# Kernel tuning notes

Hardware: AMD Instinct MI355X
Metric: run time of the kernel (lower is better)

## Reference

```python
import jax, jax.numpy as jnp
import numpy as np

EMBED_DIM = 1024
HEADS = 16
HD = EMBED_DIM // HEADS

def setup_inputs() -> dict:
    key = jax.random.key(0)
    ks = jax.random.split(key, 6)
    s = 1.0 / np.sqrt(EMBED_DIM)
    x = jax.random.normal(ks[0], (4, 2048, EMBED_DIM), dtype=jnp.float32)
    Wq = jax.random.uniform(ks[1], (EMBED_DIM, EMBED_DIM), jnp.float32, -s, s)
    Wk = jax.random.uniform(ks[2], (EMBED_DIM, EMBED_DIM), jnp.float32, -s, s)
    Wv = jax.random.uniform(ks[3], (EMBED_DIM, EMBED_DIM), jnp.float32, -s, s)
    Wo = jax.random.uniform(ks[4], (EMBED_DIM, EMBED_DIM), jnp.float32, -s, s)
    bo = jax.random.uniform(ks[5], (EMBED_DIM,), jnp.float32, -s, s)
    return {"x": x, "Wq": Wq, "Wk": Wk, "Wv": Wv, "Wo": Wo, "bo": bo}

def reference(x, Wq, Wk, Wv, Wo, bo):
    B, S, E = x.shape
    # projections (torch Linear: y = x @ W.T), split into heads -> [B,H,S,hd]
    def proj(W):
        return (x @ W.T).reshape(B, S, HEADS, HD).transpose(0, 2, 1, 3)
    q, k, v = proj(Wq), proj(Wk), proj(Wv)
    energy = jnp.einsum('bhid,bhjd->bhij', q, k) / np.sqrt(HD).astype(np.float32)
    causal = jnp.tril(jnp.ones((S, S), dtype=bool))
    energy = jnp.where(causal, energy, -jnp.inf)
    attn = jax.nn.softmax(energy, axis=-1)  # dropout omitted (eval mode)
    out = jnp.einsum('bhij,bhjd->bhid', attn, v)
    out = out.transpose(0, 2, 1, 3).reshape(B, S, E)
    return out @ Wo.T + bo
```

## Files before the change

kernel.cpp:

```cpp
#include <hip/hip_runtime.h>
#include <math.h>

#define EMB   1024
#define HEADS 16
#define HD    64
#define SEQ   2048
#define BATCH 4
#define MTOT  (BATCH * SEQ)
#define XSZ   ((size_t)MTOT * EMB)
#define WSZ   ((size_t)EMB * EMB)

typedef __attribute__((ext_vector_type(8))) short s16x8;
typedef __attribute__((ext_vector_type(4))) short s16x4;
typedef __attribute__((ext_vector_type(4))) float f32x4;

__device__ __forceinline__ short f2bf(float f) {
    unsigned u = __builtin_bit_cast(unsigned, f);
    u += 0x7fffu + ((u >> 16) & 1u);
    return (short)(u >> 16);
}

__device__ __forceinline__ unsigned pk_bf16(float a, float b) {
#if __has_builtin(__builtin_amdgcn_cvt_pk_bf16_f32)
    typedef __attribute__((ext_vector_type(2))) __bf16 bf16x2;
    return __builtin_bit_cast(unsigned, __builtin_amdgcn_cvt_pk_bf16_f32(a, b));
#else
    return (unsigned)(unsigned short)f2bf(a) |
           ((unsigned)(unsigned short)f2bf(b) << 16);
#endif
}

__device__ __forceinline__ float fexp2(float x) {
#if __has_builtin(__builtin_amdgcn_exp2f)
    return __builtin_amdgcn_exp2f(x);
#else
    return exp2f(x);
#endif
}

__device__ __forceinline__ void async16(const void* g, void* l) {
    __builtin_amdgcn_global_load_lds(
        (const __attribute__((address_space(1))) unsigned*)g,
        (__attribute__((address_space(3))) unsigned*)l, 16, 0, 0);
}

__global__ __launch_bounds__(256)
void cvt_inputs(const float* __restrict__ x,  const float* __restrict__ wq,
                const float* __restrict__ wk, const float* __restrict__ wv,
                const float* __restrict__ wo, short* __restrict__ xb,
                short* __restrict__ wcat)
{
    const size_t e = ((size_t)blockIdx.x * 256 + threadIdx.x) * 8;
    const float* src;
    short* dst;
    float scale = 1.0f;
    if (e < XSZ) {
        src = x + e;
        dst = xb + e;
    } else {
        const size_t r = e - XSZ;
        const int w = (int)(r >> 20);
        const size_t off = r & (WSZ - 1);
        src = (w == 0 ? wq : w == 1 ? wk : w == 2 ? wv : wo) + off;
        dst = wcat + r;
        if (w == 0) scale = 0.125f * 1.44269504f;
    }
    const float4 a = ((const float4*)src)[0];
    const float4 b = ((const float4*)src)[1];
    s16x8 v;
    v[0] = f2bf(a.x * scale); v[1] = f2bf(a.y * scale);
    v[2] = f2bf(a.z * scale); v[3] = f2bf(a.w * scale);
    v[4] = f2bf(b.x * scale); v[5] = f2bf(b.y * scale);
    v[6] = f2bf(b.z * scale); v[7] = f2bf(b.w * scale);
    *(s16x8*)dst = v;
}

#define BAR() __builtin_amdgcn_s_barrier()
#define WAIT_LGKM() do { asm volatile("s_waitcnt lgkmcnt(0)" ::: "memory"); \
                         __builtin_amdgcn_sched_barrier(0); } while (0)
#define WAIT_VM(n) asm volatile("s_waitcnt vmcnt(" #n ")" ::: "memory")

#define RD_A4(bA) \
    _Pragma("unroll") for (int mi = 0; mi < 4; ++mi) \
    _Pragma("unroll") for (int kk = 0; kk < 2; ++kk) \
        a[mi][kk] = *(const s16x8*)((bA) + (wm4 + mi) * 2048 + kk * 1024 + abase);

#define RD_B2(bB, hf, breg) \
    _Pragma("unroll") for (int ni = 0; ni < 2; ++ni) \
    _Pragma("unroll") for (int kk = 0; kk < 2; ++kk) \
        breg[ni][kk] = *(const s16x8*)((bB) + (wn4 + (hf) * 2 + ni) * 2048 + kk * 1024 + abase);

#define MFMA16(hf, breg) \
    __builtin_amdgcn_s_setprio(1); \
    _Pragma("unroll") for (int mi = 0; mi < 4; ++mi) \
    _Pragma("unroll") for (int ni = 0; ni < 2; ++ni) \
    _Pragma("unroll") for (int kk = 0; kk < 2; ++kk) \
        acc[mi][(hf) * 2 + ni] = __builtin_amdgcn_mfma_f32_16x16x32_bf16( \
            a[mi][kk], breg[ni][kk], acc[mi][(hf) * 2 + ni], 0, 0, 0); \
    __builtin_amdgcn_s_setprio(0);

#define STA(pM, ldsM, h, k0) do { \
    async16((pM) + (size_t)((h) * 128) * K + (k0),      (ldsM) + (h) * 16384 + wv1024); \
    async16((pM) + (size_t)((h) * 128 + 64) * K + (k0), (ldsM) + (h) * 16384 + 8192 + wv1024); \
} while (0)

#define STB(pM, ldsM, k0) do { \
    async16((pM) + (k0),                (ldsM) + wv1024); \
    async16((pM) + (size_t)64 * K + (k0), (ldsM) + 8192 + wv1024); \
} while (0)

template<bool OUT_BF16>
__global__ __launch_bounds__(512, 2)
void gemm_qp(const short* __restrict__ A, const short* __restrict__ B,
             void* __restrict__ C, int ldc, const float* __restrict__ bias,
             int K)
{
    __shared__ __align__(16) char lds[147456];

    const int tid   = threadIdx.x;
    const int wv    = tid >> 6;
    const int lane  = tid & 63;
    const int col16 = lane & 15;
    const int quad  = lane >> 4;
    const int wm    = wv >> 1;
    const int wn    = wv & 1;
    const int wm4   = wm * 4;
    const int wn4   = wn * 4;
    const int wv1024 = wv << 10;

    const int nwg = gridDim.x * gridDim.y;
    int wg = blockIdx.y * gridDim.x + blockIdx.x;
    wg = (wg & 7) * (nwg >> 3) + (wg >> 3);
    const int rowBase = (wg / gridDim.x) * 256;
    const int colBase = (wg % gridDim.x) * 128;

    const int abase = (col16 * 64 + quad * 16) ^ ((col16 & 8) << 2);

    const int rlane = (lane >> 2) & 15;
    const int rw0   = ((wv >> 1) << 4) + rlane;
    const int colSt = ((wv & 1) << 5) + (((lane & 3) << 3) ^ ((lane & 32) >> 1));
    const short* pA = A + (size_t)(rowBase + rw0) * K + colSt;
    const short* pB = B + (size_t)(colBase + rw0) * K + colSt;

    s16x8 a[4][2], bq0[2][2], bq1[2][2];
    f32x4 acc[4][4];
#pragma unroll
    for (int i = 0; i < 4; ++i)
#pragma unroll
        for (int j = 0; j < 4; ++j) acc[i][j] = (f32x4){0.f, 0.f, 0.f, 0.f};

    const int NT = K >> 6;

    char* r0 = lds;
    char* r1 = lds + 49152;
    char* r2 = lds + 98304;

    STA(pA, r0, 0, 0);  STA(pA, r0, 1, 0);  STB(pB, r0 + 32768, 0);
    STA(pA, r1, 0, 64); STA(pA, r1, 1, 64); STB(pB, r1 + 32768, 64);
    WAIT_VM(6);
    BAR();

    for (int kt = 0; kt < NT; ++kt) {
        const int k0 = kt << 6;
        const bool more = (kt + 2 < NT);

        RD_A4(r0);
        RD_B2(r0 + 32768, 0, bq0);
        if (more) { STA(pA, r2, 0, k0 + 128); STB(pB, r2 + 32768, k0 + 128); }
        BAR(); WAIT_LGKM();
        MFMA16(0, bq0);
        BAR();

        RD_B2(r0 + 32768, 1, bq1);
        if (more) STA(pA, r2, 1, k0 + 128);
        BAR(); WAIT_LGKM();
        MFMA16(1, bq1);
        if (more) { WAIT_VM(6); } else { WAIT_VM(0); }
        BAR();

        char* t = r0; r0 = r1; r1 = r2; r2 = t;
    }

    if (OUT_BF16) {
        short* Cb = (short*)C;
#pragma unroll
        for (int mi = 0; mi < 4; ++mi) {
            const int rg0 = rowBase + wm * 64 + mi * 16 + quad * 4;
#pragma unroll
            for (int ni = 0; ni < 4; ++ni) {
                const int cg = colBase + wn * 64 + ni * 16 + col16;
                const f32x4 v = acc[mi][ni];
#pragma unroll
                for (int r = 0; r < 4; ++r)
                    Cb[(size_t)(rg0 + r) * ldc + cg] = f2bf(v[r]);
            }
        }
    } else {
        float* Cf = (float*)C;
#pragma unroll
        for (int ni = 0; ni < 4; ++ni) {
            const int cg = colBase + wn * 64 + ni * 16 + col16;
            const float bj = bias ? bias[cg] : 0.f;
#pragma unroll
            for (int mi = 0; mi < 4; ++mi) {
                const int rg0 = rowBase + wm * 64 + mi * 16 + quad * 4;
                const f32x4 v = acc[mi][ni];
#pragma unroll
                for (int r = 0; r < 4; ++r)
                    Cf[(size_t)(rg0 + r) * ldc + cg] = v[r] + bj;
            }
        }
    }
}

#define LDQ 3072
__global__ __launch_bounds__(512)
void attn_mfma(const short* __restrict__ QKV, short* __restrict__ O)
{
    __shared__ short lK[64 * 72];
    __shared__ short lV[64 * 72];
    __shared__ short lP[8 * 32 * 72];

    const int tid  = threadIdx.x;
    const int wv   = tid >> 6;
    const int lane = tid & 63;
    const int col  = lane & 15;
    const int quad = lane >> 4;

    const int bh = blockIdx.y;
    const int b  = bh >> 4;
    const int h  = bh & 15;
    const size_t baseq = (size_t)b * SEQ * LDQ + (size_t)h * HD;
    const size_t basek = baseq + 1024;
    const size_t basev = baseq + 2048;
    const size_t baseo = (size_t)b * SEQ * EMB + (size_t)h * HD;

    const int krow = tid >> 3;
    const int kc0  = (tid & 7) * 8;
    short* pwave = &lP[(wv * 32) * 72];

    const s16x8 onesv = {0x3F80, 0x3F80, 0x3F80, 0x3F80,
                         0x3F80, 0x3F80, 0x3F80, 0x3F80};

    for (int half = 0; half < 2; ++half) {
        const int qsuper = half ? (7 - (int)blockIdx.x) : (int)blockIdx.x;
        const int qb = qsuper * 256;
        const int qlo_w = qb + wv * 32;

        s16x8 qf[2][2];
#pragma unroll
        for (int rb = 0; rb < 2; ++rb) {
            const short* qr = QKV + baseq + (size_t)(qlo_w + rb * 16 + col) * LDQ;
            qf[rb][0] = *(const s16x8*)(qr + quad * 8);
            qf[rb][1] = *(const s16x8*)(qr + 32 + quad * 8);
        }

        f32x4 of[2][4], lsum[2];
#pragma unroll
        for (int rb = 0; rb < 2; ++rb) {
#pragma unroll
            for (int u = 0; u < 4; ++u) of[rb][u] = (f32x4){0.f, 0.f, 0.f, 0.f};
            lsum[rb] = (f32x4){0.f, 0.f, 0.f, 0.f};
        }

        const int nt = qb / 64 + 4;

        s16x8 pk = *(const s16x8*)(QKV + basek + (size_t)krow * LDQ + kc0);
        s16x8 pv = *(const s16x8*)(QKV + basev + (size_t)lane * LDQ + wv * 8);

        for (int kt = 0; kt < nt; ++kt) {
            const int kb = kt * 64;
            __syncthreads();
            *(s16x8*)&lK[krow * 72 + kc0] = pk;
#pragma unroll
            for (int t = 0; t < 8; ++t)
                lV[(wv * 8 + t) * 72 + lane] = pv[t];
            __syncthreads();

            if (kt + 1 < nt) {
                pk = *(const s16x8*)(QKV + basek + (size_t)(kb + 64 + krow) * LDQ + kc0);
                pv = *(const s16x8*)(QKV + basev + (size_t)(kb + 64 + lane) * LDQ + wv * 8);
            }

            if (kb > qlo_w + 31) continue;

            s16x8 kf[4][2];
#pragma unroll
            for (int t = 0; t < 4; ++t) {
                kf[t][0] = *(const s16x8*)&lK[(t * 16 + col) * 72 + quad * 8];
                kf[t][1] = *(const s16x8*)&lK[(t * 16 + col) * 72 + 32 + quad * 8];
            }

#pragma unroll
            for (int rb = 0; rb < 2; ++rb) {
                const int qlo = qlo_w + rb * 16;
                const int qg  = qlo + col;

                f32x4 s[4];
#pragma unroll
                for (int t = 0; t < 4; ++t) {
                    f32x4 acc = (f32x4){0.f, 0.f, 0.f, 0.f};
                    acc = __builtin_amdgcn_mfma_f32_16x16x32_bf16(kf[t][0], qf[rb][0], acc, 0, 0, 0);
                    acc = __builtin_amdgcn_mfma_f32_16x16x32_bf16(kf[t][1], qf[rb][1], acc, 0, 0, 0);
                    s[t] = acc;
                }

                if (kb + 63 > qlo) {
#pragma unroll
                    for (int t = 0; t < 4; ++t)
#pragma unroll
                        for (int rr = 0; rr < 4; ++rr) {
                            const int kg = kb + t * 16 + quad * 4 + rr;
                            if (kg > qg) s[t][rr] = -3.0e38f;
                        }
                }

                short* pbase = pwave + (rb * 16) * 72;
#pragma unroll
                for (int t = 0; t < 4; ++t) {
                    uint2 pkd;
                    pkd.x = pk_bf16(fexp2(s[t][0]), fexp2(s[t][1]));
                    pkd.y = pk_bf16(fexp2(s[t][2]), fexp2(s[t][3]));
                    *(uint2*)&pbase[col * 72 + t * 16 + quad * 4] = pkd;
                }
            }

#pragma unroll
            for (int c = 0; c < 2; ++c) {
                s16x8 vf[4];
#pragma unroll
                for (int u = 0; u < 4; ++u)
                    vf[u] = *(const s16x8*)&lV[(u * 16 + col) * 72 + c * 32 + quad * 8];
#pragma unroll
                for (int rb = 0; rb < 2; ++rb) {
                    const s16x8 pa = *(const s16x8*)&pwave[(rb * 16 + col) * 72 + c * 32 + quad * 8];
                    lsum[rb] = __builtin_amdgcn_mfma_f32_16x16x32_bf16(onesv, pa, lsum[rb], 0, 0, 0);
#pragma unroll
                    for (int u = 0; u < 4; ++u)
                        of[rb][u] = __builtin_amdgcn_mfma_f32_16x16x32_bf16(vf[u], pa, of[rb][u], 0, 0, 0);
                }
            }
        }

#pragma unroll
        for (int rb = 0; rb < 2; ++rb) {
            const float rl = 1.f / lsum[rb][0];
            short* orow = O + baseo + (size_t)(qlo_w + rb * 16 + col) * EMB + quad * 4;
#pragma unroll
            for (int u = 0; u < 4; ++u) {
                uint2 pkd;
                pkd.x = pk_bf16(of[rb][u][0] * rl, of[rb][u][1] * rl);
                pkd.y = pk_bf16(of[rb][u][2] * rl, of[rb][u][3] * rl);
                *(uint2*)&orow[u * 16] = pkd;
            }
        }
    }
}

extern "C" void kernel_launch(void* const* d_in, const int* in_sizes, int n_in,
                              void* d_out, int out_size, void* d_ws, size_t ws_size,
                              hipStream_t stream)
{
    const float* x  = (const float*)d_in[0];
    const float* Wq = (const float*)d_in[1];
    const float* Wk = (const float*)d_in[2];
    const float* Wv = (const float*)d_in[3];
    const float* Wo = (const float*)d_in[4];
    const float* bo = (const float*)d_in[5];
    float* out = (float*)d_out;

    short* xb   = (short*)d_ws;
    short* wcat = xb + XSZ;
    short* qkv  = wcat + 4 * WSZ;
    short* ob   = qkv + (size_t)MTOT * 3 * EMB;

    const int cvt_blocks = (int)((XSZ + 4 * WSZ) / 8 / 256);
    cvt_inputs<<<cvt_blocks, 256, 0, stream>>>(x, Wq, Wk, Wv, Wo, xb, wcat);

    gemm_qp<true><<<dim3(3072 / 128, MTOT / 256), 512, 0, stream>>>(
        xb, wcat, qkv, 3072, nullptr, EMB);

    attn_mfma<<<dim3(4, BATCH * HEADS), 512, 0, stream>>>(qkv, ob);

    gemm_qp<false><<<dim3(EMB / 128, MTOT / 256), 512, 0, stream>>>(
        ob, wcat + (size_t)3 * WSZ, out, EMB, bo, EMB);
}
```

Before: 243.9 us.

## Split attention q-superblocks across blocks, swizzle LDS, and reorder block scheduling

The attention kernel previously looped over two q-superblocks per block. It now launches twice as many blocks, each handling one superblock, with a linear block-index remap so the long and short causal tiles are scheduled in a balanced order. LDS padding (stride 72) is replaced with an XOR-swizzled 128-byte row layout, which shrinks shared memory and aims to avoid bank conflicts. Launch bounds now request 4 blocks per CU, which raises occupancy but may limit registers.

```diff
diff --git a/kernel.cpp b/kernel.cpp
--- a/kernel.cpp
+++ b/kernel.cpp
@@ -214,20 +214,31 @@
 }
 
 #define LDQ 3072
-__global__ __launch_bounds__(512)
+__global__ __launch_bounds__(512, 4)
 void attn_mfma(const short* __restrict__ QKV, short* __restrict__ O)
 {
-    __shared__ short lK[64 * 72];
-    __shared__ short lV[64 * 72];
-    __shared__ short lP[8 * 32 * 72];
+    __shared__ short lK[64 * 64];
+    __shared__ short lV[64 * 64];
+    __shared__ short lP[8 * 32 * 64];
+
+    char* lKc = (char*)lK;
+    char* lVc = (char*)lV;
+    char* lPc = (char*)lP;
 
     const int tid  = threadIdx.x;
     const int wv   = tid >> 6;
     const int lane = tid & 63;
     const int col  = lane & 15;
     const int quad = lane >> 4;
-
-    const int bh = blockIdx.y;
+    const int csw  = (col & 7) << 4;
+
+    const int linear = (int)blockIdx.y * 8 + (int)blockIdx.x;
+    const int hlf = linear >> 8;
+    const int r9  = linear & 255;
+    const int bh  = (hlf << 5) + (r9 >> 3);
+    const int xr  = r9 & 7;
+    const int qsuper = hlf ? (7 - xr) : xr;
+
     const int b  = bh >> 4;
     const int h  = bh & 15;
     const size_t baseq = (size_t)b * SEQ * LDQ + (size_t)h * HD;
@@ -236,123 +247,120 @@
     const size_t baseo = (size_t)b * SEQ * EMB + (size_t)h * HD;
 
     const int krow = tid >> 3;
-    const int kc0  = (tid & 7) * 8;
-    short* pwave = &lP[(wv * 32) * 72];
+    const int kwoff = krow * 128 + ((((tid & 7) * 16)) ^ ((krow & 7) << 4));
+    char* pwv = lPc + wv * 4096;
 
     const s16x8 onesv = {0x3F80, 0x3F80, 0x3F80, 0x3F80,
                          0x3F80, 0x3F80, 0x3F80, 0x3F80};
 
-    for (int half = 0; half < 2; ++half) {
-        const int qsuper = half ? (7 - (int)blockIdx.x) : (int)blockIdx.x;
-        const int qb = qsuper * 256;
-        const int qlo_w = qb + wv * 32;
-
-        s16x8 qf[2][2];
+    const int qb = qsuper * 256;
+    const int qlo_w = qb + wv * 32;
+
+    s16x8 qf[2][2];
+#pragma unroll
+    for (int rb = 0; rb < 2; ++rb) {
+        const short* qr = QKV + baseq + (size_t)(qlo_w + rb * 16 + col) * LDQ;
+        qf[rb][0] = *(const s16x8*)(qr + quad * 8);
+        qf[rb][1] = *(const s16x8*)(qr + 32 + quad * 8);
+    }
+
+    f32x4 of[2][4], lsum[2];
+#pragma unroll
+    for (int rb = 0; rb < 2; ++rb) {
+#pragma unroll
+        for (int u = 0; u < 4; ++u) of[rb][u] = (f32x4){0.f, 0.f, 0.f, 0.f};
+        lsum[rb] = (f32x4){0.f, 0.f, 0.f, 0.f};
+    }
+
+    const int nt = qb / 64 + 4;
+
+    s16x8 pk = *(const s16x8*)(QKV + basek + (size_t)krow * LDQ + (tid & 7) * 8);
+    s16x8 pv = *(const s16x8*)(QKV + basev + (size_t)lane * LDQ + wv * 8);
+
+    for (int kt = 0; kt < nt; ++kt) {
+        const int kb = kt * 64;
+        __syncthreads();
+        *(s16x8*)(lKc + kwoff) = pk;
+#pragma unroll
+        for (int t = 0; t < 8; ++t)
+            *(short*)(lVc + (wv * 8 + t) * 128 + ((lane * 2) ^ (t << 4))) = pv[t];
+        __syncthreads();
+
+        if (kt + 1 < nt) {
+            pk = *(const s16x8*)(QKV + basek + (size_t)(kb + 64 + krow) * LDQ + (tid & 7) * 8);
+            pv = *(const s16x8*)(QKV + basev + (size_t)(kb + 64 + lane) * LDQ + wv * 8);
+        }
+
+        if (kb > qlo_w + 31) continue;
+
+        s16x8 kf[4][2];
+#pragma unroll
+        for (int t = 0; t < 4; ++t) {
+            kf[t][0] = *(const s16x8*)(lKc + (t * 16 + col) * 128 + ((quad * 16) ^ csw));
+            kf[t][1] = *(const s16x8*)(lKc + (t * 16 + col) * 128 + ((64 + quad * 16) ^ csw));
+        }
+
 #pragma unroll
         for (int rb = 0; rb < 2; ++rb) {
-            const short* qr = QKV + baseq + (size_t)(qlo_w + rb * 16 + col) * LDQ;
-            qf[rb][0] = *(const s16x8*)(qr + quad * 8);
-            qf[rb][1] = *(const s16x8*)(qr + 32 + quad * 8);
-        }
-
-        f32x4 of[2][4], lsum[2];
-#pragma unroll
-        for (int rb = 0; rb < 2; ++rb) {
-#pragma unroll
-            for (int u = 0; u < 4; ++u) of[rb][u] = (f32x4){0.f, 0.f, 0.f, 0.f};
-            lsum[rb] = (f32x4){0.f, 0.f, 0.f, 0.f};
-        }
-
-        const int nt = qb / 64 + 4;
-
-        s16x8 pk = *(const s16x8*)(QKV + basek + (size_t)krow * LDQ + kc0);
-        s16x8 pv = *(const s16x8*)(QKV + basev + (size_t)lane * LDQ + wv * 8);
-
-        for (int kt = 0; kt < nt; ++kt) {
-            const int kb = kt * 64;
-            __syncthreads();
-            *(s16x8*)&lK[krow * 72 + kc0] = pk;
-#pragma unroll
-            for (int t = 0; t < 8; ++t)
-                lV[(wv * 8 + t) * 72 + lane] = pv[t];
-            __syncthreads();
-
-            if (kt + 1 < nt) {
-                pk = *(const s16x8*)(QKV + basek + (size_t)(kb + 64 + krow) * LDQ + kc0);
-                pv = *(const s16x8*)(QKV + basev + (size_t)(kb + 64 + lane) * LDQ + wv * 8);
-            }
-
-            if (kb > qlo_w + 31) continue;
-
-            s16x8 kf[4][2];
+            const int qlo = qlo_w + rb * 16;
+            const int qg  = qlo + col;
+
+            f32x4 s[4];
 #pragma unroll
             for (int t = 0; t < 4; ++t) {
-                kf[t][0] = *(const s16x8*)&lK[(t * 16 + col) * 72 + quad * 8];
-                kf[t][1] = *(const s16x8*)&lK[(t * 16 + col) * 72 + 32 + quad * 8];
-            }
-
+                f32x4 acc = (f32x4){0.f, 0.f, 0.f, 0.f};
+                acc = __builtin_amdgcn_mfma_f32_16x16x32_bf16(kf[t][0], qf[rb][0], acc, 0, 0, 0);
+                acc = __builtin_amdgcn_mfma_f32_16x16x32_bf16(kf[t][1], qf[rb][1], acc, 0, 0, 0);
+                s[t] = acc;
+            }
+
+            if (kb + 63 > qlo) {
+#pragma unroll
+                for (int t = 0; t < 4; ++t)
+#pragma unroll
+                    for (int rr = 0; rr < 4; ++rr) {
+                        const int kg = kb + t * 16 + quad * 4 + rr;
+                        if (kg > qg) s[t][rr] = -3.0e38f;
+                    }
+            }
+
+            char* pb = pwv + (rb * 16 + col) * 128;
+#pragma unroll
+            for (int t = 0; t < 4; ++t) {
+                uint2 pkd;
+                pkd.x = pk_bf16(fexp2(s[t][0]), fexp2(s[t][1]));
+                pkd.y = pk_bf16(fexp2(s[t][2]), fexp2(s[t][3]));
+                *(uint2*)(pb + ((t * 32 + quad * 8) ^ csw)) = pkd;
+            }
+        }
+
+#pragma unroll
+        for (int c = 0; c < 2; ++c) {
+            s16x8 vf[4];
+#pragma unroll
+            for (int u = 0; u < 4; ++u)
+                vf[u] = *(const s16x8*)(lVc + (u * 16 + col) * 128 + ((c * 64 + quad * 16) ^ csw));
 #pragma unroll
             for (int rb = 0; rb < 2; ++rb) {
-                const int qlo = qlo_w + rb * 16;
-                const int qg  = qlo + col;
-
-                f32x4 s[4];
-#pragma unroll
-                for (int t = 0; t < 4; ++t) {
-                    f32x4 acc = (f32x4){0.f, 0.f, 0.f, 0.f};
-                    acc = __builtin_amdgcn_mfma_f32_16x16x32_bf16(kf[t][0], qf[rb][0], acc, 0, 0, 0);
-                    acc = __builtin_amdgcn_mfma_f32_16x16x32_bf16(kf[t][1], qf[rb][1], acc, 0, 0, 0);
-                    s[t] = acc;
-                }
-
-                if (kb + 63 > qlo) {
-#pragma unroll
-                    for (int t = 0; t < 4; ++t)
-#pragma unroll
-                        for (int rr = 0; rr < 4; ++rr) {
-                            const int kg = kb + t * 16 + quad * 4 + rr;
-                            if (kg > qg) s[t][rr] = -3.0e38f;
-                        }
-                }
-
-                short* pbase = pwave + (rb * 16) * 72;
-#pragma unroll
-                for (int t = 0; t < 4; ++t) {
-                    uint2 pkd;
-                    pkd.x = pk_bf16(fexp2(s[t][0]), fexp2(s[t][1]));
-                    pkd.y = pk_bf16(fexp2(s[t][2]), fexp2(s[t][3]));
-                    *(uint2*)&pbase[col * 72 + t * 16 + quad * 4] = pkd;
-                }
-            }
-
-#pragma unroll
-            for (int c = 0; c < 2; ++c) {
-                s16x8 vf[4];
+                const s16x8 pa = *(const s16x8*)(pwv + (rb * 16 + col) * 128 + ((c * 64 + quad * 16) ^ csw));
+                lsum[rb] = __builtin_amdgcn_mfma_f32_16x16x32_bf16(onesv, pa, lsum[rb], 0, 0, 0);
 #pragma unroll
                 for (int u = 0; u < 4; ++u)
-                    vf[u] = *(const s16x8*)&lV[(u * 16 + col) * 72 + c * 32 + quad * 8];
-#pragma unroll
-                for (int rb = 0; rb < 2; ++rb) {
-                    const s16x8 pa = *(const s16x8*)&pwave[(rb * 16 + col) * 72 + c * 32 + quad * 8];
-                    lsum[rb] = __builtin_amdgcn_mfma_f32_16x16x32_bf16(onesv, pa, lsum[rb], 0, 0, 0);
-#pragma unroll
-                    for (int u = 0; u < 4; ++u)
-                        of[rb][u] = __builtin_amdgcn_mfma_f32_16x16x32_bf16(vf[u], pa, of[rb][u], 0, 0, 0);
-                }
-            }
-        }
-
-#pragma unroll
-        for (int rb = 0; rb < 2; ++rb) {
-            const float rl = 1.f / lsum[rb][0];
-            short* orow = O + baseo + (size_t)(qlo_w + rb * 16 + col) * EMB + quad * 4;
-#pragma unroll
-            for (int u = 0; u < 4; ++u) {
-                uint2 pkd;
-                pkd.x = pk_bf16(of[rb][u][0] * rl, of[rb][u][1] * rl);
-                pkd.y = pk_bf16(of[rb][u][2] * rl, of[rb][u][3] * rl);
-                *(uint2*)&orow[u * 16] = pkd;
-            }
+                    of[rb][u] = __builtin_amdgcn_mfma_f32_16x16x32_bf16(vf[u], pa, of[rb][u], 0, 0, 0);
+            }
+        }
+    }
+
+#pragma unroll
+    for (int rb = 0; rb < 2; ++rb) {
+        const float rl = 1.f / lsum[rb][0];
+        short* orow = O + baseo + (size_t)(qlo_w + rb * 16 + col) * EMB + quad * 4;
+#pragma unroll
+        for (int u = 0; u < 4; ++u) {
+            uint2 pkd;
+            pkd.x = pk_bf16(of[rb][u][0] * rl, of[rb][u][1] * rl);
+            pkd.y = pk_bf16(of[rb][u][2] * rl, of[rb][u][3] * rl);
+            *(uint2*)&orow[u * 16] = pkd;
         }
     }
 }
@@ -380,7 +388,7 @@
     gemm_qp<true><<<dim3(3072 / 128, MTOT / 256), 512, 0, stream>>>(
         xb, wcat, qkv, 3072, nullptr, EMB);
 
-    attn_mfma<<<dim3(4, BATCH * HEADS), 512, 0, stream>>>(qkv, ob);
+    attn_mfma<<<dim3(8, BATCH * HEADS), 512, 0, stream>>>(qkv, ob);
 
     gemm_qp<false><<<dim3(EMB / 128, MTOT / 256), 512, 0, stream>>>(
         ob, wcat + (size_t)3 * WSZ, out, EMB, bo, EMB);
```

After: 339.3 us. 39.1% more time.
